# Optimization experiments

Hardware: AMD Instinct MI355X
Metric: run time of the kernel (lower is better)

The kernel has to match this reference:

```python
import jax, jax.numpy as jnp
import numpy as np

NUM_HEADS = 12


def setup_inputs() -> dict:
    key = jax.random.key(0)
    k1, k2, k3 = jax.random.split(key, 3)
    B, N, C = 2, 2048, 768
    x = jax.random.normal(k1, (B, N, C), dtype=jnp.float32)
    w_qkv = jax.random.normal(k2, (C, 3 * C), dtype=jnp.float32) * 0.02
    w_proj = jax.random.normal(k3, (C, C), dtype=jnp.float32) * 0.02
    b_proj = jnp.zeros((C,), dtype=jnp.float32)
    return {"x": x, "w_qkv": w_qkv, "w_proj": w_proj, "b_proj": b_proj}


def reference(x, w_qkv, w_proj, b_proj):
    B, N, C = x.shape
    H = NUM_HEADS
    D = C // H
    qkv = (x @ w_qkv).reshape(B, N, 3, H, D)  # [B,N,3,H,D]
    q = jnp.transpose(qkv[:, :, 0], (0, 2, 1, 3))  # [B,H,N,D]
    k = jnp.transpose(qkv[:, :, 1], (0, 2, 1, 3))
    v = jnp.transpose(qkv[:, :, 2], (0, 2, 1, 3))
    # ELU+1 feature map (note: self.scale is unused in the original forward)
    q = jax.nn.elu(q) + 1.0
    k = jax.nn.elu(k) + 1.0
    attn = jnp.einsum("bhnd,bhmd->bhnm", q, k)  # explicit O(N^2) as in source
    attn = attn / jnp.sum(attn, axis=-1, keepdims=True)
    out = jnp.einsum("bhnm,bhmd->bhnd", attn, v)  # [B,H,N,D]
    out = jnp.transpose(out, (0, 2, 1, 3)).reshape(B, N, C)
    out = out @ w_proj + b_proj
    return out, attn
```

## Files before the change

### kernel.cpp

```cpp
#include <hip/hip_runtime.h>
#include <hip/hip_bf16.h>
#include <cstdint>
#include <cmath>

#define BDIM 256

constexpr int Bb = 2;
constexpr int Nn = 2048;
constexpr int Cc = 768;
constexpr int Hh = 12;
constexpr int Dd = 64;
constexpr int TC = 3 * Cc;
constexpr int BH = Bb * Hh;
constexpr int NCHUNK = 16;
constexpr int CHROWS = Nn / NCHUNK;

typedef __attribute__((ext_vector_type(8))) short short8v;
typedef __attribute__((ext_vector_type(4))) float f32x4;

__device__ __forceinline__ float elu1(float x) {
  return x > 0.f ? x + 1.f : expf(x);
}

__device__ __forceinline__ unsigned short f2bf(float f) {
  uint32_t u = __float_as_uint(f);
  uint32_t r = (u + 0x7fff + ((u >> 16) & 1)) >> 16;
  return (unsigned short)r;
}
__device__ __forceinline__ float bf2f(unsigned short h) {
  return __uint_as_float(((uint32_t)h) << 16);
}

__device__ __forceinline__ void gll16(const unsigned short* g, unsigned short* ldsbase) {
  __builtin_amdgcn_global_load_lds((const __attribute__((address_space(1))) void*)g,
                                   (__attribute__((address_space(3))) void*)ldsbase,
                                   16, 0, 0);
}

constexpr int XBLK = 3072;
constexpr int WQBLK = (TC / 32) * (Cc / 32);
constexpr int WPBLK = (Cc / 32) * (Cc / 32);

__device__ __forceinline__ void castT_tile(const float* __restrict__ W,
                                           unsigned short* __restrict__ Wh,
                                           int K, int N, int n0, int k0, int tid,
                                           float (*t)[33]) {
  const int r = tid >> 3, c4 = (tid & 7) * 4;
  float4 v = *(const float4*)&W[(size_t)(k0 + r) * N + n0 + c4];
  t[r][c4 + 0] = v.x;
  t[r][c4 + 1] = v.y;
  t[r][c4 + 2] = v.z;
  t[r][c4 + 3] = v.w;
  __syncthreads();
  const int n = tid >> 3, k4 = (tid & 7) * 4;
  ushort4 h;
  h.x = f2bf(t[k4 + 0][n]);
  h.y = f2bf(t[k4 + 1][n]);
  h.z = f2bf(t[k4 + 2][n]);
  h.w = f2bf(t[k4 + 3][n]);
  *(ushort4*)&Wh[(size_t)(n0 + n) * K + k0 + k4] = h;
}

__global__ __launch_bounds__(BDIM) void fused_cast(const float* __restrict__ x,
                                                   const float* __restrict__ w_qkv,
                                                   const float* __restrict__ w_proj,
                                                   unsigned short* __restrict__ xh,
                                                   unsigned short* __restrict__ wqh,
                                                   unsigned short* __restrict__ wph) {
  __shared__ float t[32][33];
  const int bid = blockIdx.x, tid = threadIdx.x;
  if (bid < XBLK) {
    int i = (bid * BDIM + tid) * 4;
    float4 v = *(const float4*)&x[i];
    ushort4 h;
    h.x = f2bf(v.x);
    h.y = f2bf(v.y);
    h.z = f2bf(v.z);
    h.w = f2bf(v.w);
    *(ushort4*)&xh[i] = h;
  } else if (bid < XBLK + WQBLK) {
    int q = bid - XBLK;
    castT_tile(w_qkv, wqh, Cc, TC, (q % (TC / 32)) * 32, (q / (TC / 32)) * 32, tid, t);
  } else {
    int p = bid - XBLK - WQBLK;
    castT_tile(w_proj, wph, Cc, Cc, (p % (Cc / 32)) * 32, (p / (Cc / 32)) * 32, tid, t);
  }
}

template <int EP>
__global__ __launch_bounds__(BDIM) void mfma_k(
    const unsigned short* __restrict__ A, const unsigned short* __restrict__ Bt,
    const float* __restrict__ bias, const float* __restrict__ denom,
    float* __restrict__ C, int Mrows, int Nw, int K,
    long sAz, long sBz, long sCz,
    float* __restrict__ qp, float* __restrict__ kp, float* __restrict__ vp,
    unsigned short* __restrict__ qpb, unsigned short* __restrict__ kpb) {
  __shared__ __align__(16) unsigned short lds[16384];
  __shared__ float dnls[128];

  const int z = blockIdx.z;
  const unsigned short* A0 = A + (size_t)z * sAz;
  const unsigned short* B0 = Bt + (size_t)z * sBz;
  float* Cz = C + (size_t)z * sCz;

  const int tid = threadIdx.x;
  const int wave = tid >> 6, lane = tid & 63;
  const int wr = wave >> 1, wc = wave & 1;
  const int row0 = blockIdx.y * 128, col0 = blockIdx.x * 128;
  const int l15 = lane & 15, l4 = lane >> 4;
  const int srow = wave * 16 + (lane >> 2);
  const int scol = (lane & 3) * 8;
  const int wbase = wave * 512;

  float dnv_reg = 0.f;
  if constexpr (EP == 1) dnv_reg = denom[(size_t)z * Mrows + row0 + (tid & 127)];

  auto STAGE = [&](int buf, int k0) {
    unsigned short* dst = lds + buf * 8192 + wbase;
    gll16(&A0[(size_t)(row0 + srow) * K + k0 + scol], dst);
    gll16(&A0[(size_t)(row0 + 64 + srow) * K + k0 + scol], dst + 2048);
    gll16(&B0[(size_t)(col0 + srow) * K + k0 + scol], dst + 4096);
    gll16(&B0[(size_t)(col0 + 64 + srow) * K + k0 + scol], dst + 6144);
  };

  f32x4 acc[4][4];
#pragma unroll
  for (int i = 0; i < 4; ++i)
#pragma unroll
    for (int j = 0; j < 4; ++j) acc[i][j] = {0.f, 0.f, 0.f, 0.f};

  auto COMPUTE = [&](int buf) {
    const unsigned short* la = lds + buf * 8192;
    const unsigned short* lb = la + 4096;
    short8v av[4], bv[4];
#pragma unroll
    for (int i = 0; i < 4; ++i)
      av[i] = *(const short8v*)&la[(wr * 64 + i * 16 + l15) * 32 + l4 * 8];
#pragma unroll
    for (int j = 0; j < 4; ++j)
      bv[j] = *(const short8v*)&lb[(wc * 64 + j * 16 + l15) * 32 + l4 * 8];
#pragma unroll
    for (int i = 0; i < 4; ++i)
#pragma unroll
      for (int j = 0; j < 4; ++j)
        acc[i][j] = __builtin_amdgcn_mfma_f32_16x16x32_bf16(av[i], bv[j], acc[i][j], 0, 0, 0);
  };

  const int nt = K >> 5;
  STAGE(0, 0);
  if (nt > 1) STAGE(1, 32);
  int cur = 0;
  for (int t = 0; t < nt; ++t) {
    if (t < nt - 1)
      asm volatile("s_waitcnt vmcnt(4)" ::: "memory");
    else
      asm volatile("s_waitcnt vmcnt(0)" ::: "memory");
    __builtin_amdgcn_s_barrier();
    COMPUTE(cur);
    if (t < nt - 2) {
      __builtin_amdgcn_s_barrier();
      STAGE(cur, (t + 2) * 32);
    }
    cur ^= 1;
  }

  if constexpr (EP == 0) {
#pragma unroll
    for (int i = 0; i < 4; ++i) {
      const int rbase = row0 + wr * 64 + i * 16 + l4 * 4;
#pragma unroll
      for (int j = 0; j < 4; ++j) {
        const int col = col0 + wc * 64 + j * 16 + l15;
        float bs = bias[col];
#pragma unroll
        for (int r = 0; r < 4; ++r)
          Cz[(size_t)(rbase + r) * Nw + col] = acc[i][j][r] + bs;
      }
    }
  } else if constexpr (EP == 1) {
    if (tid < 128) dnls[tid] = 1.0f / dnv_reg;
    float* fl = (float*)lds;
#pragma unroll
    for (int i = 0; i < 4; ++i) {
      __syncthreads();
#pragma unroll
      for (int j = 0; j < 4; ++j)
#pragma unroll
        for (int r = 0; r < 4; ++r)
          fl[(wr * 16 + l4 * 4 + r) * 132 + wc * 64 + j * 16 + l15] =
              acc[i][j][r] * dnls[wr * 64 + i * 16 + l4 * 4 + r];
      __syncthreads();
#pragma unroll
      for (int p = 0; p < 4; ++p) {
        int f4 = p * 256 + tid;
        int cr = f4 >> 5, c4 = (f4 & 31) * 4;
        float4 v = *(float4*)&fl[cr * 132 + c4];
        int grow = row0 + (cr >> 4) * 64 + i * 16 + (cr & 15);
        *(float4*)&Cz[(size_t)grow * Nw + col0 + c4] = v;
      }
    }
  } else {
    const int colblk = blockIdx.x;
    const int tt = colblk / 6;
    const int rcbase = (colblk % 6) * 128 + wc * 64;
#pragma unroll
    for (int i = 0; i < 4; ++i) {
      const int rowb = row0 + wr * 64 + i * 16 + l4 * 4;
#pragma unroll
      for (int j = 0; j < 4; ++j) {
        const int rc = rcbase + j * 16 + l15;
        const int h = rc >> 6, d = rc & 63;
#pragma unroll
        for (int r = 0; r < 4; ++r) {
          const int row = rowb + r;
          const int b = row >> 11, n = row & (Nn - 1);
          const size_t idx = ((size_t)(b * Hh + h) * Nn + n) * 64 + d;
          float val = acc[i][j][r];
          if (tt == 0) {
            float e = elu1(val);
            qp[idx] = e;
            qpb[idx] = f2bf(e);
          } else if (tt == 1) {
            float e = elu1(val);
            kp[idx] = e;
            kpb[idx] = f2bf(e);
          } else {
            vp[idx] = val;
          }
        }
      }
    }
  }
}

__global__ __launch_bounds__(BDIM) void kv_partial(const float* __restrict__ kp,
                                                   const float* __restrict__ vp,
                                                   float* __restrict__ kvpart,
                                                   float* __restrict__ kspart) {
  const int chunk = blockIdx.x, bh = blockIdx.y;
  __shared__ float ks[8][64];
  __shared__ float vs[8][64];
  const int tid = threadIdx.x;
  const int nn = tid >> 5, f2 = (tid & 31) << 1;
  const int e = tid & 63, dg = tid >> 6;
  float acc[16] = {};
  float ksacc = 0.f;
  const int n0base = chunk * CHROWS;
  for (int s = 0; s < CHROWS; s += 8) {
    int n = n0base + s + nn;
    float2 k2 = *(const float2*)&kp[(size_t)(bh * Nn + n) * 64 + f2];
    float2 v2 = *(const float2*)&vp[(size_t)(bh * Nn + n) * 64 + f2];
    __syncthreads();
    *(float2*)&ks[nn][f2] = k2;
    *(float2*)&vs[nn][f2] = v2;
    __syncthreads();
#pragma unroll
    for (int j = 0; j < 8; ++j) {
      float vv = vs[j][e];
#pragma unroll
      for (int d = 0; d < 16; ++d) acc[d] += ks[j][dg * 16 + d] * vv;
      if (tid < 64) ksacc += ks[j][tid];
    }
  }
  float* outp = kvpart + (size_t)(bh * NCHUNK + chunk) * 4096;
#pragma unroll
  for (int d = 0; d < 16; ++d) outp[(dg * 16 + d) * 64 + e] = acc[d];
  if (tid < 64) kspart[(bh * NCHUNK + chunk) * 64 + tid] = ksacc;
}

__global__ __launch_bounds__(BDIM) void kv_reduce(const float* __restrict__ kvpart,
                                                  const float* __restrict__ kspart,
                                                  float* __restrict__ kv,
                                                  float* __restrict__ ksum) {
  const int seg = blockIdx.x, bh = blockIdx.y, tid = threadIdx.x;
  const int idx = seg * 256 + tid;
  float s = 0.f;
#pragma unroll 4
  for (int c = 0; c < NCHUNK; ++c) s += kvpart[(size_t)(bh * NCHUNK + c) * 4096 + idx];
  kv[(size_t)bh * 4096 + idx] = s;
  if (tid < 4) {
    int e = seg * 4 + tid;
    float s2 = 0.f;
#pragma unroll 4
    for (int c = 0; c < NCHUNK; ++c) s2 += kspart[(bh * NCHUNK + c) * 64 + e];
    ksum[bh * 64 + e] = s2;
  }
}

__global__ __launch_bounds__(BDIM) void outpre_kernel(const float* __restrict__ qp,
                                                      const float* __restrict__ kv,
                                                      const float* __restrict__ ksum,
                                                      float* __restrict__ denom,
                                                      unsigned short* __restrict__ oph) {
  const int nc = blockIdx.x, bh = blockIdx.y;
  const int b = bh / Hh, h = bh % Hh;
  __shared__ float KVs[4096];
  __shared__ float Qs2[4096];
  __shared__ float kss[64];
  __shared__ float dnv[64];
  const int tid = threadIdx.x;
  const int n0 = nc * 64;
  if (tid < 64) kss[tid] = ksum[bh * 64 + tid];
#pragma unroll
  for (int it = 0; it < 4; ++it) {
    int i = it * 1024 + tid * 4;
    *(float4*)&KVs[i] = *(const float4*)&kv[(size_t)bh * 4096 + i];
    *(float4*)&Qs2[i] = *(const float4*)&qp[(size_t)(bh * Nn + n0) * 64 + i];
  }
  __syncthreads();
  if (tid < 64) {
    float s = 0.f;
#pragma unroll
    for (int d = 0; d < 64; ++d) s += Qs2[tid * 64 + d] * kss[d];
    denom[bh * Nn + n0 + tid] = s;
    dnv[tid] = 1.0f / s;
  }
  __syncthreads();
  const int c = tid & 63, rg = tid >> 6;
  for (int j = 0; j < 16; ++j) {
    int r = rg * 16 + j;
    float s = 0.f;
#pragma unroll
    for (int d = 0; d < 64; ++d) s += Qs2[r * 64 + d] * KVs[d * 64 + c];
    int ng = n0 + r;
    size_t idx = ((size_t)b * Nn + ng) * Cc + h * Dd + c;
    oph[idx] = f2bf(s * dnv[r]);
  }
}

extern "C" void kernel_launch(void* const* d_in, const int* in_sizes, int n_in,
                              void* d_out, int out_size, void* d_ws, size_t ws_size,
                              hipStream_t stream) {
  const float* x = (const float*)d_in[0];
  const float* w_qkv = (const float*)d_in[1];
  const float* w_proj = (const float*)d_in[2];
  const float* b_proj = (const float*)d_in[3];
  float* out = (float*)d_out;
  float* attn = out + (size_t)Bb * Nn * Cc;

  float* ws = (float*)d_ws;
  float* vp = ws;
  float* qp = vp + 3145728;
  float* kp = qp + 3145728;
  float* kvpart = kp + 3145728;
  float* kspart = kvpart + 1572864;
  float* kvm = kspart + 24576;
  float* ksum = kvm + 98304;
  float* denom = ksum + 2048;
  unsigned short* us = (unsigned short*)(denom + 49152);
  unsigned short* xh = us;
  unsigned short* wqh = xh + 3145728;
  unsigned short* qpb = wqh + 1769472;
  unsigned short* kpb = qpb + 3145728;
  unsigned short* oph = kpb + 3145728;
  unsigned short* wph = oph + 3145728;

  fused_cast<<<dim3(XBLK + WQBLK + WPBLK), BDIM, 0, stream>>>(x, w_qkv, w_proj, xh, wqh,
                                                              wph);
  mfma_k<2><<<dim3(TC / 128, 32, 1), BDIM, 0, stream>>>(
      xh, wqh, nullptr, nullptr, nullptr, Bb * Nn, TC, Cc, 0, 0, 0,
      qp, kp, vp, qpb, kpb);
  kv_partial<<<dim3(NCHUNK, BH), BDIM, 0, stream>>>(kp, vp, kvpart, kspart);
  kv_reduce<<<dim3(16, BH), BDIM, 0, stream>>>(kvpart, kspart, kvm, ksum);
  outpre_kernel<<<dim3(Nn / 64, BH), BDIM, 0, stream>>>(qp, kvm, ksum, denom, oph);
  mfma_k<1><<<dim3(Nn / 128, Nn / 128, BH), BDIM, 0, stream>>>(
      qpb, kpb, nullptr, denom, attn, Nn, Nn, Dd,
      (long)Nn * Dd, (long)Nn * Dd, (long)Nn * Nn,
      nullptr, nullptr, nullptr, nullptr, nullptr);
  mfma_k<0><<<dim3(Cc / 128, 32, 1), BDIM, 0, stream>>>(
      oph, wph, b_proj, nullptr, out, Bb * Nn, Cc, Cc, 0, 0, 0,
      nullptr, nullptr, nullptr, nullptr, nullptr);
}
```

Before: 184.0 us.

## Compute Q·KV output with bf16 MFMA and drop fp32 Q buffer

Replaces the scalar fp32 LDS-based Q·KV and denominator kernel with an MFMA kernel that reads bf16 Q and a transposed bf16 KV matrix written by kv_reduce. The QKV GEMM epilogue no longer writes the fp32 Q copy, which cuts global writes and reads. The denominator is now computed from bf16 Q values, and the numerator uses bf16 KV, so precision drops compared with fp32.

```diff
diff --git a/kernel.cpp b/kernel.cpp
--- a/kernel.cpp
+++ b/kernel.cpp
@@ -93,7 +93,7 @@
     const float* __restrict__ bias, const float* __restrict__ denom,
     float* __restrict__ C, int Mrows, int Nw, int K,
     long sAz, long sBz, long sCz,
-    float* __restrict__ qp, float* __restrict__ kp, float* __restrict__ vp,
+    float* __restrict__ kp, float* __restrict__ vp,
     unsigned short* __restrict__ qpb, unsigned short* __restrict__ kpb) {
   __shared__ __align__(16) unsigned short lds[16384];
   __shared__ float dnls[128];
@@ -217,9 +217,7 @@
           const size_t idx = ((size_t)(b * Hh + h) * Nn + n) * 64 + d;
           float val = acc[i][j][r];
           if (tt == 0) {
-            float e = elu1(val);
-            qp[idx] = e;
-            qpb[idx] = f2bf(e);
+            qpb[idx] = f2bf(elu1(val));
           } else if (tt == 1) {
             float e = elu1(val);
             kp[idx] = e;
@@ -270,14 +268,15 @@
 
 __global__ __launch_bounds__(BDIM) void kv_reduce(const float* __restrict__ kvpart,
                                                   const float* __restrict__ kspart,
-                                                  float* __restrict__ kv,
+                                                  unsigned short* __restrict__ kvtb,
                                                   float* __restrict__ ksum) {
   const int seg = blockIdx.x, bh = blockIdx.y, tid = threadIdx.x;
   const int idx = seg * 256 + tid;
   float s = 0.f;
 #pragma unroll 4
   for (int c = 0; c < NCHUNK; ++c) s += kvpart[(size_t)(bh * NCHUNK + c) * 4096 + idx];
-  kv[(size_t)bh * 4096 + idx] = s;
+  const int dk = idx >> 6, dv = idx & 63;
+  kvtb[(size_t)bh * 4096 + dv * 64 + dk] = f2bf(s);
   if (tid < 4) {
     int e = seg * 4 + tid;
     float s2 = 0.f;
@@ -287,44 +286,78 @@
   }
 }
 
-__global__ __launch_bounds__(BDIM) void outpre_kernel(const float* __restrict__ qp,
-                                                      const float* __restrict__ kv,
-                                                      const float* __restrict__ ksum,
-                                                      float* __restrict__ denom,
-                                                      unsigned short* __restrict__ oph) {
+__global__ __launch_bounds__(BDIM) void outpre_mfma(
+    const unsigned short* __restrict__ qpb, const unsigned short* __restrict__ kvtb,
+    const float* __restrict__ ksum, float* __restrict__ denom,
+    unsigned short* __restrict__ oph) {
   const int nc = blockIdx.x, bh = blockIdx.y;
   const int b = bh / Hh, h = bh % Hh;
-  __shared__ float KVs[4096];
-  __shared__ float Qs2[4096];
   __shared__ float kss[64];
-  __shared__ float dnv[64];
+  __shared__ float dnls[128];
   const int tid = threadIdx.x;
-  const int n0 = nc * 64;
+  const int wv = tid >> 6, lane = tid & 63;
+  const int l15 = lane & 15, l4 = lane >> 4;
   if (tid < 64) kss[tid] = ksum[bh * 64 + tid];
-#pragma unroll
-  for (int it = 0; it < 4; ++it) {
-    int i = it * 1024 + tid * 4;
-    *(float4*)&KVs[i] = *(const float4*)&kv[(size_t)bh * 4096 + i];
-    *(float4*)&Qs2[i] = *(const float4*)&qp[(size_t)(bh * Nn + n0) * 64 + i];
-  }
+
+  const int rowb = nc * 128 + wv * 32;
+  const unsigned short* Aq = qpb + ((size_t)bh * Nn + rowb) * 64;
+  const unsigned short* Bk = kvtb + (size_t)bh * 4096;
+
+  short8v av[2][2], bv[4][2];
+#pragma unroll
+  for (int ks = 0; ks < 2; ++ks) {
+#pragma unroll
+    for (int i = 0; i < 2; ++i)
+      av[i][ks] = *(const short8v*)&Aq[(size_t)(i * 16 + l15) * 64 + ks * 32 + l4 * 8];
+#pragma unroll
+    for (int j = 0; j < 4; ++j)
+      bv[j][ks] = *(const short8v*)&Bk[(size_t)(j * 16 + l15) * 64 + ks * 32 + l4 * 8];
+  }
+  f32x4 acc[2][4];
+#pragma unroll
+  for (int i = 0; i < 2; ++i)
+#pragma unroll
+    for (int j = 0; j < 4; ++j) acc[i][j] = {0.f, 0.f, 0.f, 0.f};
+#pragma unroll
+  for (int ks = 0; ks < 2; ++ks)
+#pragma unroll
+    for (int i = 0; i < 2; ++i)
+#pragma unroll
+      for (int j = 0; j < 4; ++j)
+        acc[i][j] = __builtin_amdgcn_mfma_f32_16x16x32_bf16(av[i][ks], bv[j][ks],
+                                                            acc[i][j], 0, 0, 0);
+
   __syncthreads();
-  if (tid < 64) {
-    float s = 0.f;
-#pragma unroll
-    for (int d = 0; d < 64; ++d) s += Qs2[tid * 64 + d] * kss[d];
-    denom[bh * Nn + n0 + tid] = s;
-    dnv[tid] = 1.0f / s;
+  float dpart[2] = {0.f, 0.f};
+#pragma unroll
+  for (int ks = 0; ks < 2; ++ks)
+#pragma unroll
+    for (int i = 0; i < 2; ++i)
+#pragma unroll
+      for (int t = 0; t < 8; ++t)
+        dpart[i] += bf2f((unsigned short)av[i][ks][t]) * kss[ks * 32 + l4 * 8 + t];
+#pragma unroll
+  for (int i = 0; i < 2; ++i) {
+    dpart[i] += __shfl_xor(dpart[i], 16);
+    dpart[i] += __shfl_xor(dpart[i], 32);
+    if (l4 == 0) {
+      dnls[wv * 32 + i * 16 + l15] = dpart[i];
+      denom[(size_t)bh * Nn + rowb + i * 16 + l15] = dpart[i];
+    }
   }
   __syncthreads();
-  const int c = tid & 63, rg = tid >> 6;
-  for (int j = 0; j < 16; ++j) {
-    int r = rg * 16 + j;
-    float s = 0.f;
-#pragma unroll
-    for (int d = 0; d < 64; ++d) s += Qs2[r * 64 + d] * KVs[d * 64 + c];
-    int ng = n0 + r;
-    size_t idx = ((size_t)b * Nn + ng) * Cc + h * Dd + c;
-    oph[idx] = f2bf(s * dnv[r]);
+#pragma unroll
+  for (int i = 0; i < 2; ++i) {
+#pragma unroll
+    for (int r = 0; r < 4; ++r) {
+      const int rl = i * 16 + l4 * 4 + r;
+      const float rd = 1.0f / dnls[wv * 32 + rl];
+      const int nrow = rowb + rl;
+#pragma unroll
+      for (int j = 0; j < 4; ++j)
+        oph[((size_t)b * Nn + nrow) * Cc + h * 64 + j * 16 + l15] =
+            f2bf(acc[i][j][r] * rd);
+    }
   }
 }
 
@@ -340,34 +373,33 @@
 
   float* ws = (float*)d_ws;
   float* vp = ws;
-  float* qp = vp + 3145728;
-  float* kp = qp + 3145728;
+  float* kp = vp + 3145728;
   float* kvpart = kp + 3145728;
   float* kspart = kvpart + 1572864;
-  float* kvm = kspart + 24576;
-  float* ksum = kvm + 98304;
+  float* ksum = kspart + 24576;
   float* denom = ksum + 2048;
   unsigned short* us = (unsigned short*)(denom + 49152);
   unsigned short* xh = us;
   unsigned short* wqh = xh + 3145728;
   unsigned short* qpb = wqh + 1769472;
   unsigned short* kpb = qpb + 3145728;
-  unsigned short* oph = kpb + 3145728;
+  unsigned short* kvtb = kpb + 3145728;
+  unsigned short* oph = kvtb + 98304;
   unsigned short* wph = oph + 3145728;
 
   fused_cast<<<dim3(XBLK + WQBLK + WPBLK), BDIM, 0, stream>>>(x, w_qkv, w_proj, xh, wqh,
                                                               wph);
   mfma_k<2><<<dim3(TC / 128, 32, 1), BDIM, 0, stream>>>(
       xh, wqh, nullptr, nullptr, nullptr, Bb * Nn, TC, Cc, 0, 0, 0,
-      qp, kp, vp, qpb, kpb);
+      kp, vp, qpb, kpb);
   kv_partial<<<dim3(NCHUNK, BH), BDIM, 0, stream>>>(kp, vp, kvpart, kspart);
-  kv_reduce<<<dim3(16, BH), BDIM, 0, stream>>>(kvpart, kspart, kvm, ksum);
-  outpre_kernel<<<dim3(Nn / 64, BH), BDIM, 0, stream>>>(qp, kvm, ksum, denom, oph);
+  kv_reduce<<<dim3(16, BH), BDIM, 0, stream>>>(kvpart, kspart, kvtb, ksum);
+  outpre_mfma<<<dim3(Nn / 128, BH), BDIM, 0, stream>>>(qpb, kvtb, ksum, denom, oph);
   mfma_k<1><<<dim3(Nn / 128, Nn / 128, BH), BDIM, 0, stream>>>(
       qpb, kpb, nullptr, denom, attn, Nn, Nn, Dd,
       (long)Nn * Dd, (long)Nn * Dd, (long)Nn * Nn,
-      nullptr, nullptr, nullptr, nullptr, nullptr);
+      nullptr, nullptr, nullptr, nullptr);
   mfma_k<0><<<dim3(Cc / 128, 32, 1), BDIM, 0, stream>>>(
       oph, wph, b_proj, nullptr, out, Bb * Nn, Cc, Cc, 0, 0, 0,
-      nullptr, nullptr, nullptr, nullptr, nullptr);
-}
+      nullptr, nullptr, nullptr, nullptr);
+}
```

Result: faster. 171.3 us (-6.9%).
